# Kernel optimization log

Hardware: AMD Instinct MI355X
Metric: run time of the kernel (lower is better)

Reference implementation:

```python
import jax, jax.numpy as jnp
import numpy as np


def setup_inputs() -> dict:
    key = jax.random.key(0)
    ks = jax.random.split(key, 24)
    N, E, D, A = 50000, 600000, 128, 128   # nodes, edges, in_dim(=out_dim), attn_dim
    NQ, NREL = 1024, 200
    NRE = 2 * NREL + 1                      # rela_embed rows
    s = 0.05

    def nrm(k, shape):
        return jax.random.normal(k, shape, jnp.float32) * s

    # edges columns: [query_idx, unused, rel, unused, sub, obj]
    r_idx = jax.random.randint(ks[0], (E,), 0, NQ, jnp.int32)
    rel = jax.random.randint(ks[1], (E,), 0, NRE, jnp.int32)
    sub = jax.random.randint(ks[2], (E,), 0, N, jnp.int32)
    # guarantee every node appears as an obj so the softmax denominator is never 0
    obj = jnp.concatenate([jnp.arange(N, dtype=jnp.int32),
                           jax.random.randint(ks[3], (E - N,), 0, N, jnp.int32)])
    zc = jnp.zeros((E,), jnp.int32)
    edges = jnp.stack([r_idx, zc, rel, zc, sub, obj], axis=1)

    q_rel = jax.random.randint(ks[4], (NQ,), 0, NRE, jnp.int32)
    hidden = jax.random.normal(ks[5], (N, D), jnp.float32)

    return {
        "hidden": hidden,
        "rela_embed": nrm(ks[6], (NRE, D)),
        # GateUnit (GRU-style gate over x=[h_r; h_qr] with state h_s)
        "Wz": nrm(ks[7], (2 * D, D)), "Uz": nrm(ks[8], (D, D)), "bz": jnp.zeros((D,), jnp.float32),
        "Wr_g": nrm(ks[9], (2 * D, D)), "Ur": nrm(ks[10], (D, D)), "br": jnp.zeros((D,), jnp.float32),
        "Whh": nrm(ks[11], (2 * D, D)), "Uh": nrm(ks[12], (D, D)), "bh": jnp.zeros((D,), jnp.float32),
        # attention
        "Ws_attn": nrm(ks[13], (D, A)),
        "Wqr_attn": nrm(ks[14], (D, A)), "b_qr": jnp.zeros((A,), jnp.float32),
        "w_alpha": nrm(ks[15], (A, 1)), "b_alpha": jnp.zeros((1,), jnp.float32),
        # output projection
        "W_h": nrm(ks[16], (D, D)),
        "q_rel": q_rel,
        "edges": edges,
        "n_node": N,
    }


def gate_unit(h_r, h_qr, h_s, Wz, Uz, bz, Wr_g, Ur, br, Whh, Uh, bh):
    # GRU-style gated update: x = [h_r; h_qr], state = h_s
    x = jnp.concatenate([h_r, h_qr], axis=-1)
    z = jax.nn.sigmoid(x @ Wz + h_s @ Uz + bz)
    r = jax.nn.sigmoid(x @ Wr_g + h_s @ Ur + br)
    h_tilde = jnp.tanh(x @ Whh + (r * h_s) @ Uh + bh)
    return (1.0 - z) * h_s + z * h_tilde


def reference(hidden, rela_embed, Wz, Uz, bz, Wr_g, Ur, br, Whh, Uh, bh,
              Ws_attn, Wqr_attn, b_qr, w_alpha, b_alpha, W_h,
              q_rel, edges, n_node):
    r_idx = edges[:, 0]   # query index per edge
    rel = edges[:, 2]
    sub = edges[:, 4]
    obj = edges[:, 5]

    h_s = hidden[sub]               # [E, D] gather
    h_r = rela_embed[rel]           # [E, D]
    hq = rela_embed[q_rel]          # [NQ, D]
    h_qr = hq[r_idx]                # [E, D]

    # node_group[obj] = r_idx (duplicate writes: last-write semantics, as torch)
    node_group = jnp.zeros((n_node,), dtype=edges.dtype).at[obj].set(r_idx)
    h_n_qr = hq[node_group]         # [n_node, D]

    message = gate_unit(h_r, h_qr, h_s, Wz, Uz, bz, Wr_g, Ur, br, Whh, Uh, bh)  # [E, D]

    attn = jax.nn.relu(message @ Ws_attn + h_qr @ Wqr_attn + b_qr) @ w_alpha + b_alpha  # [E, 1]
    exp_a = jnp.exp(attn)

    sum_exp = jax.ops.segment_sum(exp_a, obj, num_segments=n_node)             # [n_node, 1]
    agg = jax.ops.segment_sum(exp_a * message, obj, num_segments=n_node)       # [n_node, D]
    message_agg = agg / sum_exp

    hidden_new = jax.nn.relu(message_agg @ W_h)
    return hidden_new, h_n_qr
```

## Files before the change

kernel.cpp:

```cpp
#include <hip/hip_runtime.h>
#include <hip/hip_bf16.h>

#define D 128

typedef unsigned int u32;
typedef unsigned short ushort_t;

typedef __attribute__((ext_vector_type(8))) __bf16 bf16x8;
typedef __attribute__((ext_vector_type(4))) float f32x4;

__device__ __forceinline__ float bf2f(ushort_t u){ return __uint_as_float(((u32)u)<<16); }
__device__ __forceinline__ ushort_t f2bf(float f){
  u32 x = __float_as_uint(f);
  return (ushort_t)((x + 0x7fffu + ((x>>16)&1u)) >> 16);
}
__device__ __forceinline__ float2 bfp2(u32 w){
  float2 r; r.x = __uint_as_float(w<<16); r.y = __uint_as_float(w & 0xffff0000u); return r;
}
__device__ __forceinline__ u32 packbf(float a, float b){
  return (u32)f2bf(a) | ((u32)f2bf(b)<<16);
}
__device__ __forceinline__ u32 cvtpk(float a, float b){
  u32 r; asm("v_cvt_pk_bf16_f32 %0, %1, %2" : "=v"(r) : "v"(a), "v"(b)); return r;
}
__device__ __forceinline__ ushort_t cvt1(float a){
  u32 r; asm("v_cvt_pk_bf16_f32 %0, %1, %1" : "=v"(r) : "v"(a)); return (ushort_t)r;
}
__device__ __forceinline__ void atompk(ushort_t* p, u32 v){
  asm volatile("global_atomic_pk_add_bf16 %0, %1, off" :: "v"(p), "v"(v) : "memory");
}
__device__ __forceinline__ float sigm(float x){ return 1.0f/(1.0f+__expf(-x)); }
__device__ __forceinline__ float ftanh(float x){
  float e = __expf(-2.0f*fabsf(x));
  float t = (1.0f-e)/(1.0f+e);
  return copysignf(t,x);
}

__global__ void detect_kernel(const u32* __restrict__ words, int* flag){
  int t = threadIdx.x;
  int cnt = 0;
  for (int i = t; i < 512; i += 64){
    u32 w = words[i];
    u32 e = (w >> 7) & 0xFFu;
    if (e >= 100u && e <= 126u) cnt++;
  }
  #pragma unroll
  for (int off = 32; off > 0; off >>= 1) cnt += __shfl_xor(cnt, off);
  if (t == 0) *flag = (cnt < 256) ? 1 : 0;
}

struct CvtArgs { const void* src[17]; ushort_t* dst[17]; int n[17]; };

__global__ __launch_bounds__(256) void convert_kernel(CvtArgs a, const int* __restrict__ flag){
  int isf = *flag;
  int gid = blockIdx.x*blockDim.x + threadIdx.x;
  int gs  = gridDim.x*blockDim.x;
  for (int s = 0; s < 17; s++){
    int n = a.n[s];
    ushort_t* dst = a.dst[s];
    if (isf){
      const float* src = (const float*)a.src[s];
      for (int j = gid; j < n; j += gs) dst[j] = f2bf(src[j]);
    } else {
      const ushort_t* src = (const ushort_t*)a.src[s];
      for (int j = gid; j < n; j += gs) dst[j] = src[j];
    }
  }
}

__global__ void init_kernel(u32* aggz, float* sum_exp, int* last_edge, int N){
  int i = blockIdx.x*blockDim.x + threadIdx.x;
  int stride = gridDim.x*blockDim.x;
  int na = N*D/2;
  for (int j=i; j<na; j+=stride) aggz[j]=0u;
  for (int j=i; j<N;  j+=stride){ sum_exp[j]=0.f; last_edge[j]=-1; }
}

__global__ void table_kernel(const ushort_t* __restrict__ rela,
  const ushort_t* __restrict__ Wz, const ushort_t* __restrict__ Wr, const ushort_t* __restrict__ Wh,
  const ushort_t* __restrict__ Wqr,
  const ushort_t* __restrict__ bz, const ushort_t* __restrict__ br, const ushort_t* __restrict__ bh,
  const ushort_t* __restrict__ bqr,
  const int* __restrict__ q_rel,
  ushort_t* hq_tab, u32* __restrict__ RELP, u32* __restrict__ RIDP,
  ushort_t* CaT, int NRE, int NQ)
{
  __shared__ float hrow[D];
  int d = threadIdx.x;
  int b = blockIdx.x;
  if (b < NRE) {
    const ushort_t* row = rela + (size_t)b*D;
    hrow[d] = bf2f(row[d]);
    __syncthreads();
    float az=0.f, ar=0.f, ah=0.f;
    for (int k=0;k<D;k++){
      float h = hrow[k];
      az += h*bf2f(Wz[k*D+d]);
      ar += h*bf2f(Wr[k*D+d]);
      ah += h*bf2f(Wh[k*D+d]);
    }
    float azn = __shfl_xor(az,1), arn = __shfl_xor(ar,1), ahn = __shfl_xor(ah,1);
    if (!(d & 1)){
      u32* out = RELP + (size_t)b*192 + (d>>1)*3;
      out[0] = packbf(az, azn); out[1] = packbf(ar, arn); out[2] = packbf(ah, ahn);
    }
  } else {
    int q = b - NRE; if (q >= NQ) return;
    int rq = q_rel[q];
    const ushort_t* row = rela + (size_t)rq*D;
    hrow[d] = bf2f(row[d]);
    hq_tab[q*D+d] = row[d];
    __syncthreads();
    float vz=bf2f(bz[d]), vr=bf2f(br[d]), vh=bf2f(bh[d]), vc=bf2f(bqr[d]);
    for (int k=0;k<D;k++){
      float h = hrow[k];
      vz += h*bf2f(Wz[(D+k)*D+d]);
      vr += h*bf2f(Wr[(D+k)*D+d]);
      vh += h*bf2f(Wh[(D+k)*D+d]);
      vc += h*bf2f(Wqr[k*D+d]);
    }
    float vzn = __shfl_xor(vz,1), vrn = __shfl_xor(vr,1), vhn = __shfl_xor(vh,1);
    if (!(d & 1)){
      u32* out = RIDP + (size_t)q*192 + (d>>1)*3;
      out[0] = packbf(vz, vzn); out[1] = packbf(vr, vrn); out[2] = packbf(vh, vhn);
    }
    CaT[q*D + (d&15)*8 + (d>>4)] = f2bf(vc);
  }
}

__global__ __launch_bounds__(256) void hu_kernel(const ushort_t* __restrict__ hidden,
  const ushort_t* __restrict__ Uz, const ushort_t* __restrict__ Ur,
  u32* __restrict__ SUB3, int N)
{
  int l = threadIdx.x & 63;
  int gw = (int)((blockIdx.x * blockDim.x + threadIdx.x) >> 6);
  int nw = (int)((gridDim.x * blockDim.x) >> 6);
  int c0 = 2*l;
  for (int n = gw; n < N; n += nw) {
    u32 hraw = *(const u32*)(hidden + (size_t)n*D + c0);
    float2 h = bfp2(hraw);
    float az0=0.f,az1=0.f,ar0=0.f,ar1=0.f;
    #pragma unroll 4
    for (int kp=0; kp<64; kp++) {
      float hx = __shfl(h.x, kp);
      float hy = __shfl(h.y, kp);
      float2 uz0 = bfp2(*(const u32*)(Uz + (2*kp)*D + c0));
      float2 uz1 = bfp2(*(const u32*)(Uz + (2*kp+1)*D + c0));
      float2 ur0 = bfp2(*(const u32*)(Ur + (2*kp)*D + c0));
      float2 ur1 = bfp2(*(const u32*)(Ur + (2*kp+1)*D + c0));
      az0 += hx*uz0.x + hy*uz1.x;
      az1 += hx*uz0.y + hy*uz1.y;
      ar0 += hx*ur0.x + hy*ur1.x;
      ar1 += hx*ur0.y + hy*ur1.y;
    }
    u32* out = SUB3 + (size_t)n*192 + l*3;
    out[0] = packbf(az0, az1); out[1] = packbf(ar0, ar1); out[2] = hraw;
  }
}

#define SMEM_WST 32768
#define SMEM_VA  65536
#define EDGE_SMEM (65536 + 8*8192)

__device__ __forceinline__ void matvec16(const char* vA_hi, const char* vA_lo,
                                         const char* Bm, int l, f32x4 acc[8])
{
  int arow = l & 15, agrp = l >> 4;
  int swz = (arow & 7) << 4;
  bf16x8 ah[4], al[4];
  #pragma unroll
  for (int kk=0; kk<4; kk++){
    int off = (kk*64 + agrp*16) ^ swz;
    ah[kk] = *(const bf16x8*)(vA_hi + arow*256 + off);
    al[kk] = *(const bf16x8*)(vA_lo + arow*256 + off);
  }
  #pragma unroll
  for (int t=0; t<8; t++){
    const char* bbase = Bm + (t*16 + arow)*256;
    #pragma unroll
    for (int kk=0; kk<4; kk++){
      bf16x8 bf = *(const bf16x8*)(bbase + ((kk*64 + agrp*16) ^ swz));
      acc[t] = __builtin_amdgcn_mfma_f32_16x16x32_bf16(ah[kk], bf, acc[t], 0,0,0);
      acc[t] = __builtin_amdgcn_mfma_f32_16x16x32_bf16(al[kk], bf, acc[t], 0,0,0);
    }
  }
}

__global__ __launch_bounds__(512, 2) void edge_kernel(
  const int* __restrict__ edges,
  const u32* __restrict__ SUB3, const u32* __restrict__ RELP, const u32* __restrict__ RIDP,
  const ushort_t* __restrict__ CaT,
  const ushort_t* __restrict__ Uh, const ushort_t* __restrict__ Ws,
  const ushort_t* __restrict__ w_alpha, const ushort_t* __restrict__ b_alpha,
  ushort_t* __restrict__ aggh, float* __restrict__ sum_exp, int* __restrict__ last_edge,
  int E)
{
  extern __shared__ char smem[];
  int tid = threadIdx.x;
  int w = tid >> 6, l = tid & 63;

  for (int idx = tid; idx < 128*64; idx += 512) {
    int k  = idx >> 6;
    int cp = idx & 63;
    u32 wu = *(const u32*)(Uh + (size_t)k*D + 2*cp);
    u32 ww = *(const u32*)(Ws + (size_t)k*D + 2*cp);
    int r0 = 2*cp, r1 = 2*cp+1;
    int o0 = (2*k) ^ ((r0&7)<<4);
    int o1 = (2*k) ^ ((r1&7)<<4);
    *(ushort_t*)(smem + r0*256 + o0) = (ushort_t)(wu & 0xffffu);
    *(ushort_t*)(smem + r1*256 + o1) = (ushort_t)(wu >> 16);
    *(ushort_t*)(smem + SMEM_WST + r0*256 + o0) = (ushort_t)(ww & 0xffffu);
    *(ushort_t*)(smem + SMEM_WST + r1*256 + o1) = (ushort_t)(ww >> 16);
  }
  __syncthreads();

  char* vA_hi = smem + SMEM_VA + w*8192;
  char* vA_lo = vA_hi + 4096;
  u32*  accb  = (u32*)vA_hi;

  int arow = l & 15, agrp = l >> 4;
  float wal[8];
  #pragma unroll
  for (int t=0; t<8; t++) wal[t] = bf2f(w_alpha[t*16 + arow]);
  float bal = bf2f(b_alpha[0]);
  int c0 = 2*l;

  int nIter = (E + 127) >> 7;
  for (int it = blockIdx.x; it < nIter; it += gridDim.x) {
    int eb = it*128 + w*16;

    int myE = eb + arow; if (myE >= E) myE = E - 1;
    const int* ep = edges + (size_t)myE*6;
    int v_ridx = ep[0];
    int v_rel  = ep[2];
    int v_sub  = ep[4];
    int v_obj  = ep[5];

    u32 zpk[16], hwd[16], acp[16];
    #pragma unroll
    for (int e=0; e<16; e++){
      int rel = __shfl(v_rel, e);
      int rid = __shfl(v_ridx, e);
      int sub = __shfl(v_sub, e);
      uint3 rp = *(const uint3*)(RELP + (size_t)rel*192 + l*3);
      uint3 qp = *(const uint3*)(RIDP + (size_t)rid*192 + l*3);
      uint3 sp = *(const uint3*)(SUB3 + (size_t)sub*192 + l*3);
      float2 az = bfp2(rp.x), ar = bfp2(rp.y), ah = bfp2(rp.z);
      float2 bz = bfp2(qp.x), br = bfp2(qp.y), bh = bfp2(qp.z);
      float2 hz = bfp2(sp.x), hr = bfp2(sp.y), hs = bfp2(sp.z);
      float z0 = sigm(az.x+bz.x+hz.x), z1 = sigm(az.y+bz.y+hz.y);
      float r0 = sigm(ar.x+br.x+hr.x), r1 = sigm(ar.y+br.y+hr.y);
      float v0 = r0*hs.x, v1 = r1*hs.y;
      u32 u0 = __float_as_uint(v0), u1 = __float_as_uint(v1);
      u32 whi = (u0 >> 16) | (u1 & 0xffff0000u);
      float vl0 = v0 - __uint_as_float(u0 & 0xffff0000u);
      float vl1 = v1 - __uint_as_float(u1 & 0xffff0000u);
      int voff = e*256 + ((4*l) ^ ((e&7)<<4));
      *(u32*)(vA_hi + voff) = whi;
      *(u32*)(vA_lo + voff) = cvtpk(vl0, vl1);
      zpk[e] = cvtpk(z0, z1);
      hwd[e] = sp.z;
      acp[e] = cvtpk(ah.x+bh.x, ah.y+bh.y);
    }

    f32x4 acc[8];
    #pragma unroll
    for (int t=0; t<8; t++) acc[t] = (f32x4){0.f,0.f,0.f,0.f};
    matvec16(vA_hi, vA_lo, smem, l, acc);

    #pragma unroll
    for (int t=0; t<8; t++){
      #pragma unroll
      for (int r=0; r<4; r++){
        int e_ = agrp*4 + r;
        int c  = t*16 + arow;
        accb[e_*128 + (c ^ (agrp<<3))] = __float_as_uint(acc[t][r]);
      }
    }
    float2 xv[16];
    #pragma unroll
    for (int e=0; e<16; e++)
      xv[e] = *(float2*)&accb[e*128 + ((2*l) ^ ((e>>2)<<3))];

    float mf0[16], mf1[16];
    #pragma unroll
    for (int e=0; e<16; e++){
      float2 ac = bfp2(acp[e]);
      float2 zh = bfp2(zpk[e]);
      float2 hs = bfp2(hwd[e]);
      float ht0 = ftanh(xv[e].x + ac.x);
      float ht1 = ftanh(xv[e].y + ac.y);
      float m0 = (1.0f - zh.x)*hs.x + zh.x*ht0;
      float m1 = (1.0f - zh.y)*hs.y + zh.y*ht1;
      mf0[e] = m0; mf1[e] = m1;
      u32 u0 = __float_as_uint(m0), u1 = __float_as_uint(m1);
      u32 whi = (u0 >> 16) | (u1 & 0xffff0000u);
      float vl0 = m0 - __uint_as_float(u0 & 0xffff0000u);
      float vl1 = m1 - __uint_as_float(u1 & 0xffff0000u);
      int voff = e*256 + ((4*l) ^ ((e&7)<<4));
      *(u32*)(vA_hi + voff) = whi;
      *(u32*)(vA_lo + voff) = cvtpk(vl0, vl1);
    }

    f32x4 a2[8];
    #pragma unroll
    for (int t=0; t<8; t++) a2[t] = (f32x4){0.f,0.f,0.f,0.f};
    matvec16(vA_hi, vA_lo, smem + SMEM_WST, l, a2);

    float ea[4];
    #pragma unroll
    for (int r=0; r<4; r++){
      int rid_r = __shfl(v_ridx, agrp*4 + r);
      uint4 cw = *(const uint4*)(CaT + (size_t)rid_r*D + arow*8);
      float2 c01 = bfp2(cw.x), c23 = bfp2(cw.y), c45 = bfp2(cw.z), c67 = bfp2(cw.w);
      float s = 0.f;
      s += fmaxf(a2[0][r]+c01.x,0.f)*wal[0];
      s += fmaxf(a2[1][r]+c01.y,0.f)*wal[1];
      s += fmaxf(a2[2][r]+c23.x,0.f)*wal[2];
      s += fmaxf(a2[3][r]+c23.y,0.f)*wal[3];
      s += fmaxf(a2[4][r]+c45.x,0.f)*wal[4];
      s += fmaxf(a2[5][r]+c45.y,0.f)*wal[5];
      s += fmaxf(a2[6][r]+c67.x,0.f)*wal[6];
      s += fmaxf(a2[7][r]+c67.y,0.f)*wal[7];
      s += __shfl_xor(s, 1); s += __shfl_xor(s, 2);
      s += __shfl_xor(s, 4); s += __shfl_xor(s, 8);
      ea[r] = __expf(s + bal);
    }

    #pragma unroll
    for (int e=0; e<16; e++){
      float ea_e = __shfl(ea[e & 3], (e >> 2) << 4);
      int obj_e  = __shfl(v_obj, e);
      int eg = eb + e;
      if (eg < E){
        atompk(aggh + (size_t)obj_e*D + c0, cvtpk(ea_e*mf0[e], ea_e*mf1[e]));
        if (l == e){
          atomicAdd(sum_exp + obj_e, ea_e);
          atomicMax(last_edge + obj_e, eg);
        }
      }
    }
  }
}

__global__ __launch_bounds__(256) void final_kernel(
  const ushort_t* __restrict__ aggh, const float* __restrict__ sum_exp,
  const int* __restrict__ last_edge, const int* __restrict__ edges,
  const ushort_t* __restrict__ hq_tab, const ushort_t* __restrict__ Wh,
  const int* __restrict__ flag, void* __restrict__ out_base, int N)
{
  __shared__ float mb[4][D][4];
  int tid = threadIdx.x, w = tid >> 6, l = tid & 63;
  int c0 = 2*l, c1 = c0+1;
  int isf = *flag;
  float* out0f = (float*)out_base;
  float* out1f = out0f + (size_t)N*D;
  ushort_t* out0h = (ushort_t*)out_base;
  ushort_t* out1h = out0h + (size_t)N*D;
  int nIter = (N + 15) >> 4;
  for (int it = blockIdx.x; it < nIter; it += gridDim.x){
    int base = it*16 + w*4;
    int rq[4];
    #pragma unroll
    for (int e=0;e<4;e++){
      int n = base + e; if (n >= N) n = N-1;
      float se = sum_exp[n];
      float inv = (se > 0.f) ? (1.0f/se) : 0.f;
      float2 m = bfp2(*(const u32*)(aggh + (size_t)n*D + c0));
      mb[w][c0][e] = m.x*inv; mb[w][c1][e] = m.y*inv;
      int le = last_edge[n];
      rq[e] = (le >= 0) ? edges[(size_t)le*6] : 0;
    }
    float a0[4] = {0,0,0,0}, a1[4] = {0,0,0,0};
    #pragma unroll 4
    for (int kp=0; kp<64; kp++){
      float4 ma = *(float4*)&mb[w][2*kp][0];
      float4 mv = *(float4*)&mb[w][2*kp+1][0];
      float2 u0 = bfp2(*(const u32*)(Wh + (2*kp)*D + c0));
      float2 u1 = bfp2(*(const u32*)(Wh + (2*kp+1)*D + c0));
      a0[0] += ma.x*u0.x + mv.x*u1.x;  a1[0] += ma.x*u0.y + mv.x*u1.y;
      a0[1] += ma.y*u0.x + mv.y*u1.x;  a1[1] += ma.y*u0.y + mv.y*u1.y;
      a0[2] += ma.z*u0.x + mv.z*u1.x;  a1[2] += ma.z*u0.y + mv.z*u1.y;
      a0[3] += ma.w*u0.x + mv.w*u1.x;  a1[3] += ma.w*u0.y + mv.w*u1.y;
    }
    #pragma unroll
    for (int e=0;e<4;e++){
      int n = base + e; if (n >= N) continue;
      float r0 = fmaxf(a0[e], 0.f), r1 = fmaxf(a1[e], 0.f);
      u32 hqw = *(const u32*)(hq_tab + (size_t)rq[e]*D + c0);
      if (isf){
        float2 o0; o0.x = r0; o0.y = r1;
        *(float2*)(out0f + (size_t)n*D + c0) = o0;
        float2 hv = bfp2(hqw);
        *(float2*)(out1f + (size_t)n*D + c0) = hv;
      } else {
        *(u32*)(out0h + (size_t)n*D + c0) = packbf(r0, r1);
        *(u32*)(out1h + (size_t)n*D + c0) = hqw;
      }
    }
  }
}

extern "C" void kernel_launch(void* const* d_in, const int* in_sizes, int n_in,
                              void* d_out, int out_size, void* d_ws, size_t ws_size,
                              hipStream_t stream)
{
  const int* q_rel = (const int*)d_in[17];
  const int* edges = (const int*)d_in[18];

  int N   = in_sizes[0]/D;
  int NRE = in_sizes[1]/D;
  int NQ  = in_sizes[17];
  int E   = in_sizes[18]/6;

  char* ws = (char*)d_ws;
  size_t o = 0;
  auto alloc = [&](size_t bytes)->void*{
    void* p = ws + o; o += (bytes + 255) & ~(size_t)255; return p;
  };
  ushort_t* aggh  = (ushort_t*)alloc((size_t)N*D*2);
  float* sum_exp  = (float*)alloc((size_t)N*4);
  int*   lastedge = (int*)  alloc((size_t)N*4);
  int*   flag     = (int*)  alloc(256);

  ushort_t* canon[17];
  for (int i=0;i<17;i++) canon[i] = (ushort_t*)alloc((size_t)in_sizes[i]*2);

  ushort_t* hq_tab = (ushort_t*)alloc((size_t)NQ*D*2);
  ushort_t* CaT = (ushort_t*)alloc((size_t)NQ*D*2);
  u32* RELP = (u32*)alloc((size_t)NRE*192*4);
  u32* RIDP = (u32*)alloc((size_t)NQ*192*4);
  u32* SUB3 = (u32*)alloc((size_t)N*192*4);

  CvtArgs ca;
  for (int i=0;i<17;i++){ ca.src[i]=d_in[i]; ca.dst[i]=canon[i]; ca.n[i]=in_sizes[i]; }

  const ushort_t* hidden = canon[0];
  const ushort_t* rela   = canon[1];
  const ushort_t* Wz  = canon[2];
  const ushort_t* Uz  = canon[3];
  const ushort_t* bz  = canon[4];
  const ushort_t* Wr  = canon[5];
  const ushort_t* Ur  = canon[6];
  const ushort_t* br  = canon[7];
  const ushort_t* Whh = canon[8];
  const ushort_t* Uh  = canon[9];
  const ushort_t* bh  = canon[10];
  const ushort_t* Ws  = canon[11];
  const ushort_t* Wqr = canon[12];
  const ushort_t* bqr = canon[13];
  const ushort_t* wal = canon[14];
  const ushort_t* bal = canon[15];
  const ushort_t* W_h = canon[16];

  detect_kernel<<<1, 64, 0, stream>>>((const u32*)d_in[1], flag);
  convert_kernel<<<1024, 256, 0, stream>>>(ca, flag);
  init_kernel<<<4096, 256, 0, stream>>>((u32*)aggh, sum_exp, lastedge, N);
  table_kernel<<<NRE+NQ, 128, 0, stream>>>(rela, Wz, Wr, Whh, Wqr, bz, br, bh, bqr,
                                           q_rel, hq_tab, RELP, RIDP, CaT, NRE, NQ);
  hu_kernel<<<1024, 256, 0, stream>>>(hidden, Uz, Ur, SUB3, N);

  hipFuncSetAttribute(reinterpret_cast<const void*>(edge_kernel),
                      hipFuncAttributeMaxDynamicSharedMemorySize, EDGE_SMEM);
  edge_kernel<<<256, 512, EDGE_SMEM, stream>>>(edges, SUB3, RELP, RIDP, CaT,
                                               Uh, Ws, wal, bal, aggh, sum_exp, lastedge, E);
  final_kernel<<<1024, 256, 0, stream>>>(aggh, sum_exp, lastedge, edges, hq_tab, W_h,
                                         flag, d_out, N);
}
```

Before: 727.3 us.

## Use MFMA for node-side Uz/Ur projection, vectorize convert/init, batch per-edge atomics

After: 619.3 us. 14.8% less time.

```diff
diff --git a/kernel.cpp b/kernel.cpp
--- a/kernel.cpp
+++ b/kernel.cpp
@@ -58,12 +58,23 @@
   for (int s = 0; s < 17; s++){
     int n = a.n[s];
     ushort_t* dst = a.dst[s];
+    int n4 = n >> 2;
     if (isf){
+      const float4* src4 = (const float4*)a.src[s];
+      uint2* dst4 = (uint2*)dst;
+      for (int j = gid; j < n4; j += gs){
+        float4 v = src4[j];
+        uint2 o; o.x = packbf(v.x, v.y); o.y = packbf(v.z, v.w);
+        dst4[j] = o;
+      }
       const float* src = (const float*)a.src[s];
-      for (int j = gid; j < n; j += gs) dst[j] = f2bf(src[j]);
+      for (int j = (n4<<2) + gid; j < n; j += gs) dst[j] = f2bf(src[j]);
     } else {
+      const uint2* src4 = (const uint2*)a.src[s];
+      uint2* dst4 = (uint2*)dst;
+      for (int j = gid; j < n4; j += gs) dst4[j] = src4[j];
       const ushort_t* src = (const ushort_t*)a.src[s];
-      for (int j = gid; j < n; j += gs) dst[j] = src[j];
+      for (int j = (n4<<2) + gid; j < n; j += gs) dst[j] = src[j];
     }
   }
 }
@@ -72,7 +83,10 @@
   int i = blockIdx.x*blockDim.x + threadIdx.x;
   int stride = gridDim.x*blockDim.x;
   int na = N*D/2;
-  for (int j=i; j<na; j+=stride) aggz[j]=0u;
+  int na4 = na >> 2;
+  uint4 z4 = make_uint4(0,0,0,0);
+  for (int j=i; j<na4; j+=stride) ((uint4*)aggz)[j] = z4;
+  for (int j=(na4<<2)+i; j<na; j+=stride) aggz[j]=0u;
   for (int j=i; j<N;  j+=stride){ sum_exp[j]=0.f; last_edge[j]=-1; }
 }
 
@@ -128,40 +142,6 @@
   }
 }
 
-__global__ __launch_bounds__(256) void hu_kernel(const ushort_t* __restrict__ hidden,
-  const ushort_t* __restrict__ Uz, const ushort_t* __restrict__ Ur,
-  u32* __restrict__ SUB3, int N)
-{
-  int l = threadIdx.x & 63;
-  int gw = (int)((blockIdx.x * blockDim.x + threadIdx.x) >> 6);
-  int nw = (int)((gridDim.x * blockDim.x) >> 6);
-  int c0 = 2*l;
-  for (int n = gw; n < N; n += nw) {
-    u32 hraw = *(const u32*)(hidden + (size_t)n*D + c0);
-    float2 h = bfp2(hraw);
-    float az0=0.f,az1=0.f,ar0=0.f,ar1=0.f;
-    #pragma unroll 4
-    for (int kp=0; kp<64; kp++) {
-      float hx = __shfl(h.x, kp);
-      float hy = __shfl(h.y, kp);
-      float2 uz0 = bfp2(*(const u32*)(Uz + (2*kp)*D + c0));
-      float2 uz1 = bfp2(*(const u32*)(Uz + (2*kp+1)*D + c0));
-      float2 ur0 = bfp2(*(const u32*)(Ur + (2*kp)*D + c0));
-      float2 ur1 = bfp2(*(const u32*)(Ur + (2*kp+1)*D + c0));
-      az0 += hx*uz0.x + hy*uz1.x;
-      az1 += hx*uz0.y + hy*uz1.y;
-      ar0 += hx*ur0.x + hy*ur1.x;
-      ar1 += hx*ur0.y + hy*ur1.y;
-    }
-    u32* out = SUB3 + (size_t)n*192 + l*3;
-    out[0] = packbf(az0, az1); out[1] = packbf(ar0, ar1); out[2] = hraw;
-  }
-}
-
-#define SMEM_WST 32768
-#define SMEM_VA  65536
-#define EDGE_SMEM (65536 + 8*8192)
-
 __device__ __forceinline__ void matvec16(const char* vA_hi, const char* vA_lo,
                                          const char* Bm, int l, f32x4 acc[8])
 {
@@ -185,6 +165,120 @@
     }
   }
 }
+
+__device__ __forceinline__ void matvec16s(const char* vA,
+                                          const char* Bm, int l, f32x4 acc[8])
+{
+  int arow = l & 15, agrp = l >> 4;
+  int swz = (arow & 7) << 4;
+  bf16x8 ah[4];
+  #pragma unroll
+  for (int kk=0; kk<4; kk++){
+    int off = (kk*64 + agrp*16) ^ swz;
+    ah[kk] = *(const bf16x8*)(vA + arow*256 + off);
+  }
+  #pragma unroll
+  for (int t=0; t<8; t++){
+    const char* bbase = Bm + (t*16 + arow)*256;
+    #pragma unroll
+    for (int kk=0; kk<4; kk++){
+      bf16x8 bf = *(const bf16x8*)(bbase + ((kk*64 + agrp*16) ^ swz));
+      acc[t] = __builtin_amdgcn_mfma_f32_16x16x32_bf16(ah[kk], bf, acc[t], 0,0,0);
+    }
+  }
+}
+
+#define HU_SMEM (65536 + 8*8192)
+
+__global__ __launch_bounds__(512, 2) void hu_kernel(
+  const ushort_t* __restrict__ hidden,
+  const ushort_t* __restrict__ Uz, const ushort_t* __restrict__ Ur,
+  u32* __restrict__ SUB3, int N)
+{
+  extern __shared__ char smem[];
+  int tid = threadIdx.x;
+  int w = tid >> 6, l = tid & 63;
+
+  for (int idx = tid; idx < 128*64; idx += 512) {
+    int k  = idx >> 6;
+    int cp = idx & 63;
+    u32 wu = *(const u32*)(Uz + (size_t)k*D + 2*cp);
+    u32 ww = *(const u32*)(Ur + (size_t)k*D + 2*cp);
+    int r0 = 2*cp, r1 = 2*cp+1;
+    int o0 = (2*k) ^ ((r0&7)<<4);
+    int o1 = (2*k) ^ ((r1&7)<<4);
+    *(ushort_t*)(smem + r0*256 + o0) = (ushort_t)(wu & 0xffffu);
+    *(ushort_t*)(smem + r1*256 + o1) = (ushort_t)(wu >> 16);
+    *(ushort_t*)(smem + 32768 + r0*256 + o0) = (ushort_t)(ww & 0xffffu);
+    *(ushort_t*)(smem + 32768 + r1*256 + o1) = (ushort_t)(ww >> 16);
+  }
+  __syncthreads();
+
+  char* vA  = smem + 65536 + w*8192;
+  u32* accb = (u32*)vA;
+  int arow = l & 15, agrp = l >> 4;
+  int c0 = 2*l;
+
+  int nIter = (N + 127) >> 7;
+  for (int it = blockIdx.x; it < nIter; it += gridDim.x) {
+    int base = it*128 + w*16;
+    u32 hword[16];
+    #pragma unroll
+    for (int e=0;e<16;e++){
+      int n = base + e; if (n >= N) n = N-1;
+      u32 hw = *(const u32*)(hidden + (size_t)n*D + c0);
+      hword[e] = hw;
+      *(u32*)(vA + e*256 + ((4*l) ^ ((e&7)<<4))) = hw;
+    }
+    f32x4 az[8], ar[8];
+    #pragma unroll
+    for (int t=0;t<8;t++){ az[t]=(f32x4){0.f,0.f,0.f,0.f}; ar[t]=(f32x4){0.f,0.f,0.f,0.f}; }
+    matvec16s(vA, smem, l, az);
+    matvec16s(vA, smem + 32768, l, ar);
+
+    #pragma unroll
+    for (int t=0;t<8;t++){
+      #pragma unroll
+      for (int r=0;r<4;r++){
+        int e_ = agrp*4 + r;
+        int c  = t*16 + arow;
+        accb[e_*128 + (c ^ (agrp<<3))] = __float_as_uint(az[t][r]);
+      }
+    }
+    float2 xz[16];
+    #pragma unroll
+    for (int e=0;e<16;e++)
+      xz[e] = *(float2*)&accb[e*128 + ((2*l) ^ ((e>>2)<<3))];
+    #pragma unroll
+    for (int t=0;t<8;t++){
+      #pragma unroll
+      for (int r=0;r<4;r++){
+        int e_ = agrp*4 + r;
+        int c  = t*16 + arow;
+        accb[e_*128 + (c ^ (agrp<<3))] = __float_as_uint(ar[t][r]);
+      }
+    }
+    float2 xr[16];
+    #pragma unroll
+    for (int e=0;e<16;e++)
+      xr[e] = *(float2*)&accb[e*128 + ((2*l) ^ ((e>>2)<<3))];
+
+    #pragma unroll
+    for (int e=0;e<16;e++){
+      int n = base + e;
+      if (n < N){
+        u32* out = SUB3 + (size_t)n*192 + l*3;
+        out[0] = packbf(xz[e].x, xz[e].y);
+        out[1] = packbf(xr[e].x, xr[e].y);
+        out[2] = hword[e];
+      }
+    }
+  }
+}
+
+#define SMEM_WST 32768
+#define SMEM_VA  65536
+#define EDGE_SMEM (65536 + 8*8192)
 
 __global__ __launch_bounds__(512, 2) void edge_kernel(
   const int* __restrict__ edges,
@@ -332,12 +426,20 @@
       float ea_e = __shfl(ea[e & 3], (e >> 2) << 4);
       int obj_e  = __shfl(v_obj, e);
       int eg = eb + e;
-      if (eg < E){
+      if (eg < E)
         atompk(aggh + (size_t)obj_e*D + c0, cvtpk(ea_e*mf0[e], ea_e*mf1[e]));
-        if (l == e){
-          atomicAdd(sum_exp + obj_e, ea_e);
-          atomicMax(last_edge + obj_e, eg);
-        }
+    }
+    {
+      int srcl = (arow >> 2) << 4;
+      float s0 = __shfl(ea[0], srcl);
+      float s1 = __shfl(ea[1], srcl);
+      float s2 = __shfl(ea[2], srcl);
+      float s3 = __shfl(ea[3], srcl);
+      int rr = arow & 3;
+      float eav = (rr == 0) ? s0 : (rr == 1) ? s1 : (rr == 2) ? s2 : s3;
+      if (agrp == 0 && (eb + arow) < E){
+        atomicAdd(sum_exp + v_obj, eav);
+        atomicMax(last_edge + v_obj, eb + arow);
       }
     }
   }
@@ -458,7 +560,10 @@
   init_kernel<<<4096, 256, 0, stream>>>((u32*)aggh, sum_exp, lastedge, N);
   table_kernel<<<NRE+NQ, 128, 0, stream>>>(rela, Wz, Wr, Whh, Wqr, bz, br, bh, bqr,
                                            q_rel, hq_tab, RELP, RIDP, CaT, NRE, NQ);
-  hu_kernel<<<1024, 256, 0, stream>>>(hidden, Uz, Ur, SUB3, N);
+
+  hipFuncSetAttribute(reinterpret_cast<const void*>(hu_kernel),
+                      hipFuncAttributeMaxDynamicSharedMemorySize, HU_SMEM);
+  hu_kernel<<<256, 512, HU_SMEM, stream>>>(hidden, Uz, Ur, SUB3, N);
 
   hipFuncSetAttribute(reinterpret_cast<const void*>(edge_kernel),
                       hipFuncAttributeMaxDynamicSharedMemorySize, EDGE_SMEM);
```
